# Kernel tuning notes

Measured on AMD Instinct MI355X. Metric: run time of the kernel, lower is better.

The kernel has to match this reference:

```python
import jax, jax.numpy as jnp
import numpy as np

B, H, S = 256, 128, 2048

def setup_inputs() -> dict:
    key = jax.random.key(0)
    ks = jax.random.split(key, 8)
    static_embedding = jax.random.normal(ks[0], (B, H, S), dtype=jnp.float32)
    dynamic_embedding = jax.random.normal(ks[1], (B, S, H), dtype=jnp.float32)
    decoder_output = jax.random.normal(ks[2], (B, H, 1), dtype=jnp.float32)
    mask = jax.random.randint(ks[3], (B, S), 0, 2).astype(bool)
    # xavier-uniform-ish init scales
    lim_v = float(np.sqrt(6.0 / (1 + H)))
    lim_W = float(np.sqrt(6.0 / (H + 3 * H)))
    lim_W2 = float(np.sqrt(6.0 / (H + 2 * H)))
    v = jax.random.uniform(ks[4], (H,), minval=-lim_v, maxval=lim_v, dtype=jnp.float32)
    W = jax.random.uniform(ks[5], (H, 3 * H), minval=-lim_W, maxval=lim_W, dtype=jnp.float32)
    v2 = jax.random.uniform(ks[6], (H,), minval=-lim_v, maxval=lim_v, dtype=jnp.float32)
    W2 = jax.random.uniform(ks[7], (H, 2 * H), minval=-lim_W2, maxval=lim_W2, dtype=jnp.float32)
    return {"static_embedding": static_embedding, "dynamic_embedding": dynamic_embedding,
            "decoder_output": decoder_output, "mask": mask,
            "v": v, "W": W, "v2": v2, "W2": W2}


def reference(static_embedding, dynamic_embedding, decoder_output, mask, v, W, v2, W2):
    b, h, s = static_embedding.shape
    dec = jnp.broadcast_to(decoder_output, (b, h, s))               # [B,H,S]
    hidden = jnp.concatenate(
        [static_embedding, jnp.swapaxes(dynamic_embedding, 1, 2), dec], axis=1)  # [B,3H,S]
    # stage 1: additive scoring  v^T tanh(W @ hidden)
    t1 = jnp.tanh(jnp.einsum('hk,bks->bhs', W, hidden))             # [B,H,S]
    attns = jnp.einsum('h,bhs->bs', v, t1)                          # [B,S]
    enc_attn = jax.nn.softmax(attns, axis=1)                        # [B,S]
    # context over static embeddings
    context = jnp.einsum('bs,bhs->bh', enc_attn, static_embedding)  # [B,H]
    energy = jnp.concatenate(
        [static_embedding, jnp.broadcast_to(context[:, :, None], (b, h, s))], axis=1)  # [B,2H,S]
    # stage 2
    t2 = jnp.tanh(jnp.einsum('hk,bks->bhs', W2, energy))            # [B,H,S]
    probs = jnp.einsum('h,bhs->bs', v2, t2)                         # [B,S]
    probs = jnp.where(mask, -jnp.inf, probs)
    return jax.nn.softmax(probs, axis=1)
```

## Files before the change

### kernel.cpp

```cpp
#include <hip/hip_runtime.h>
#include <stdint.h>
#include <math.h>

#define B_ 256
#define H_ 128
#define S_ 2048

typedef __attribute__((ext_vector_type(8))) short short8;
typedef __attribute__((ext_vector_type(4))) float f32x4;
typedef __attribute__((ext_vector_type(4))) unsigned int u32x4;

typedef const __attribute__((address_space(1))) void gvoid_t;
typedef __attribute__((address_space(3))) void lvoid_t;

__device__ __forceinline__ unsigned short f2bf(float f) {
  uint32_t u = __builtin_bit_cast(uint32_t, f);
  u += 0x7fffu + ((u >> 16) & 1u);
  return (unsigned short)(u >> 16);
}

__device__ __forceinline__ uint32_t cvtpk(float lo, float hi) {
  uint32_t r;
  asm("v_cvt_pk_bf16_f32 %0, %1, %2" : "=v"(r) : "v"(lo), "v"(hi));
  return r;
}

__device__ __forceinline__ float bf2f(unsigned short u) {
  return __builtin_bit_cast(float, (uint32_t)u << 16);
}

__device__ __forceinline__ float tanh5(float x) {
  float e = __builtin_amdgcn_exp2f(x * 2.8853900817779268f);
  float r = __builtin_amdgcn_rcpf(1.0f + e);
  return fmaf(-2.0f, r, 1.0f);
}

#define WS_NEED 4718592u
#define WST_OFF 8388608u
#define WS_T_NEED (WST_OFF + (size_t)B_ * (S_/16) * 4 * 64 * 8 * 2)

__global__ __launch_bounds__(256) void prep_wfrags(
    const float* __restrict__ W, const float* __restrict__ W2,
    unsigned short* __restrict__ wsA) {
  int idx = blockIdx.x * 256 + threadIdx.x;
  if (idx >= 24 * 4 * 64 * 8) return;
  int j = idx & 7;
  int lane = (idx >> 3) & 63;
  int t = (idx >> 9) & 3;
  int tile = idx >> 11;
  int li = lane & 15;
  int k = t * 32 + (lane >> 4) * 8 + j;
  float val;
  if (tile < 8)        val = W[(tile * 16 + li) * 384 + k];
  else if (tile < 16)  val = W2[((tile - 8) * 16 + li) * 256 + k];
  else                 val = W[((tile - 16) * 16 + li) * 384 + 128 + k];
  wsA[idx] = f2bf(val);
}

__global__ __launch_bounds__(128) void prep_c1(
    const float* __restrict__ W, const float* __restrict__ dec,
    float* __restrict__ c1) {
  int b = blockIdx.x;
  int h = threadIdx.x;
  __shared__ float sdec[H_];
  sdec[h] = dec[b * H_ + h];
  __syncthreads();
  const float* wr = W + h * 384 + 256;
  float acc = 0.f;
  #pragma unroll 4
  for (int k = 0; k < 128; ++k) acc += wr[k] * sdec[k];
  c1[b * H_ + h] = acc;
}

__global__ void detect_mask(const unsigned char* __restrict__ mb, int* __restrict__ flag) {
  __shared__ int sGT1, sNZ;
  if (threadIdx.x == 0) { sGT1 = 0; sNZ = 0; }
  __syncthreads();
  int gt1 = 0, nz = 0;
  for (int i = threadIdx.x; i < 8192; i += 256) {
    unsigned char c = mb[i];
    if (c > 1) gt1 = 1;
    if ((i & 3) && c) nz = 1;
  }
  if (gt1) atomicOr(&sGT1, 1);
  if (nz)  atomicOr(&sNZ, 1);
  __syncthreads();
  if (threadIdx.x == 0) *flag = sGT1 ? 2 : (sNZ ? 1 : 0);
}

__global__ __launch_bounds__(256) void stage1(
    const float* __restrict__ sEmb, const float* __restrict__ dEmb,
    const unsigned short* __restrict__ wsA, const float* __restrict__ c1,
    const float* __restrict__ v, float* __restrict__ attns,
    unsigned short* __restrict__ wsT) {
  const int b = blockIdx.y;
  const int tid = threadIdx.x;
  const int lane = tid & 63, w = tid >> 6, g = lane >> 4, li = lane & 15;
  __shared__ float sS[128 * 64];
  __shared__ unsigned short frag[4][8][512];
  __shared__ float spart[256];
  __shared__ float sc1[H_], sv[H_];

  const size_t sbase = (size_t)b * H_ * S_;
  const size_t dbase = (size_t)b * S_ * H_;
  const int sblk = blockIdx.x * 512;

  short8 aW[2][4], aB[2][4];
  #pragma unroll
  for (int mm = 0; mm < 2; ++mm)
    #pragma unroll
    for (int t = 0; t < 4; ++t) {
      aW[mm][t] = *(const short8*)(wsA + (size_t)(((2 * w + mm) * 4 + t) * 64 + lane) * 8);
      aB[mm][t] = *(const short8*)(wsA + (size_t)(((16 + 2 * w + mm) * 4 + t) * 64 + lane) * 8);
    }
  if (tid < 128) { sc1[tid] = c1[b * H_ + tid]; sv[tid] = v[tid]; }

  const int lrow = lane >> 4, lcol4 = 4 * (lane & 15);
  auto stageS = [&](int soff) {
    #pragma unroll
    for (int i = 0; i < 8; ++i) {
      int r = 32 * w + 4 * i + lrow;
      int gcol = lcol4 ^ (((r >> 3) & 3) << 3);
      const float* src = sEmb + sbase + (size_t)r * S_ + soff + gcol;
      __builtin_amdgcn_global_load_lds((gvoid_t*)src, (lvoid_t*)&sS[(32 * w + 4 * i) * 64],
                                       16, 0, 0);
    }
  };
  f32x4 dv[8];
  auto loadD = [&](int soff) {
    const float* dr = dEmb + dbase + (size_t)(soff + 16 * w + li) * H_ + 8 * g;
    #pragma unroll
    for (int t = 0; t < 4; ++t) {
      dv[2 * t]     = *(const f32x4*)(dr + 32 * t);
      dv[2 * t + 1] = *(const f32x4*)(dr + 32 * t + 4);
    }
  };

  stageS(sblk);
  loadD(sblk);

  const int colA = (16 * w + li) ^ (g << 3);

  for (int c = 0; c < 8; ++c) {
    const int soff = sblk + c * 64;
    __syncthreads();
    if (c > 0 && tid < 64)
      attns[(size_t)b * S_ + soff - 64 + tid] =
          spart[tid] + spart[64 + tid] + spart[128 + tid] + spart[192 + tid];

    #pragma unroll
    for (int t = 0; t < 4; ++t) {
      const int rb = (32 * t + 8 * g) * 64 + colA;
      uint32_t s0 = cvtpk(sS[rb], sS[rb + 64]);
      uint32_t s1 = cvtpk(sS[rb + 128], sS[rb + 192]);
      uint32_t s2 = cvtpk(sS[rb + 256], sS[rb + 320]);
      uint32_t s3 = cvtpk(sS[rb + 384], sS[rb + 448]);
      u32x4 us = {s0, s1, s2, s3};
      short8 bS = __builtin_bit_cast(short8, us);
      uint32_t d0 = cvtpk(dv[2 * t].x, dv[2 * t].y);
      uint32_t d1 = cvtpk(dv[2 * t].z, dv[2 * t].w);
      uint32_t d2 = cvtpk(dv[2 * t + 1].x, dv[2 * t + 1].y);
      uint32_t d3 = cvtpk(dv[2 * t + 1].z, dv[2 * t + 1].w);
      u32x4 ud = {d0, d1, d2, d3};
      short8 bD = __builtin_bit_cast(short8, ud);
      *(short8*)&frag[w][t][lane * 8] = bS;
      *(short8*)&frag[w][4 + t][lane * 8] = bD;
      if (wsT)
        *(short8*)&wsT[(((size_t)b * (S_ / 16) + (soff >> 4) + w) * 4 + t) * 512 + lane * 8] = bS;
    }
    __syncthreads();
    if (c + 1 < 8) { stageS(soff + 64); loadD(soff + 64); }

    f32x4 acc[4][2];
    #pragma unroll
    for (int st = 0; st < 4; ++st) { acc[st][0] = (f32x4)0.0f; acc[st][1] = (f32x4)0.0f; }
    #pragma unroll
    for (int st = 0; st < 4; ++st)
      #pragma unroll
      for (int t = 0; t < 4; ++t) {
        short8 bS = *(const short8*)&frag[st][t][lane * 8];
        short8 bD = *(const short8*)&frag[st][4 + t][lane * 8];
        acc[st][0] = __builtin_amdgcn_mfma_f32_16x16x32_bf16(aW[0][t], bS, acc[st][0], 0, 0, 0);
        acc[st][1] = __builtin_amdgcn_mfma_f32_16x16x32_bf16(aW[1][t], bS, acc[st][1], 0, 0, 0);
        acc[st][0] = __builtin_amdgcn_mfma_f32_16x16x32_bf16(aB[0][t], bD, acc[st][0], 0, 0, 0);
        acc[st][1] = __builtin_amdgcn_mfma_f32_16x16x32_bf16(aB[1][t], bD, acc[st][1], 0, 0, 0);
      }

    #pragma unroll
    for (int st = 0; st < 4; ++st) {
      float part = 0.f;
      #pragma unroll
      for (int mm = 0; mm < 2; ++mm)
        #pragma unroll
        for (int r = 0; r < 4; ++r) {
          int h = 32 * w + 16 * mm + 4 * g + r;
          part += sv[h] * tanh5(acc[st][mm][r] + sc1[h]);
        }
      part += __shfl_xor(part, 16);
      part += __shfl_xor(part, 32);
      if (lane < 16) spart[w * 64 + st * 16 + li] = part;
    }
  }
  __syncthreads();
  if (tid < 64)
    attns[(size_t)b * S_ + sblk + 448 + tid] =
        spart[tid] + spart[64 + tid] + spart[128 + tid] + spart[192 + tid];
}

__global__ __launch_bounds__(512) void fuse2(
    const float* __restrict__ attns, const unsigned short* __restrict__ wsT,
    const unsigned short* __restrict__ wsA, const float* __restrict__ W2,
    const float* __restrict__ v2, const unsigned char* __restrict__ mask8,
    const int* __restrict__ flag, float* __restrict__ out) {
  const int b = blockIdx.x;
  const int tid = threadIdx.x;
  const int lane = tid & 63, wv = tid >> 6, g = lane >> 4, li = lane & 15;
  __shared__ float buf[S_];
  __shared__ float sctx[8][H_];
  __shared__ float2 sq[H_];
  __shared__ float wred[8];
  __shared__ float sred;

  const size_t pbase = (size_t)b * (S_ / 16);

  float a[4];
  #pragma unroll
  for (int i = 0; i < 4; ++i) a[i] = attns[(size_t)b * S_ + i * 512 + tid];
  float mx = fmaxf(fmaxf(a[0], a[1]), fmaxf(a[2], a[3]));
  #pragma unroll
  for (int off = 32; off >= 1; off >>= 1) mx = fmaxf(mx, __shfl_xor(mx, off));
  if (lane == 0) wred[wv] = mx;
  __syncthreads();
  if (tid == 0) {
    float m = wred[0];
    #pragma unroll
    for (int i = 1; i < 8; ++i) m = fmaxf(m, wred[i]);
    sred = m;
  }
  __syncthreads();
  mx = sred;
  __syncthreads();
  float sum = 0.f;
  #pragma unroll
  for (int i = 0; i < 4; ++i) {
    float e = __expf(a[i] - mx);
    buf[i * 512 + tid] = e;
    sum += e;
  }
  #pragma unroll
  for (int off = 32; off >= 1; off >>= 1) sum += __shfl_xor(sum, off);
  if (lane == 0) wred[wv] = sum;
  __syncthreads();
  if (tid == 0) {
    float s = 0.f;
    #pragma unroll
    for (int i = 0; i < 8; ++i) s += wred[i];
    sred = 1.0f / s;
  }
  __syncthreads();
  const float inv1 = sred;
  __syncthreads();

  float hacc[4][8];
  #pragma unroll
  for (int t = 0; t < 4; ++t)
    #pragma unroll
    for (int j = 0; j < 8; ++j) hacc[t][j] = 0.f;
  short8 cur[4];
  #pragma unroll
  for (int t = 0; t < 4; ++t)
    cur[t] = *(const short8*)&wsT[((pbase + wv) * 4 + t) * 512 + lane * 8];
  for (int stile = wv; stile < 128; stile += 8) {
    short8 nxt[4];
    const bool more = (stile + 8) < 128;
    if (more) {
      #pragma unroll
      for (int t = 0; t < 4; ++t)
        nxt[t] = *(const short8*)&wsT[((pbase + stile + 8) * 4 + t) * 512 + lane * 8];
    }
    float pw = buf[stile * 16 + li];
    #pragma unroll
    for (int t = 0; t < 4; ++t)
      #pragma unroll
      for (int j = 0; j < 8; ++j)
        hacc[t][j] = fmaf(pw, bf2f((unsigned short)cur[t][j]), hacc[t][j]);
    if (more) {
      #pragma unroll
      for (int t = 0; t < 4; ++t) cur[t] = nxt[t];
    }
  }
  #pragma unroll
  for (int t = 0; t < 4; ++t)
    #pragma unroll
    for (int j = 0; j < 8; ++j) {
      float x = hacc[t][j];
      x += __shfl_xor(x, 1); x += __shfl_xor(x, 2);
      x += __shfl_xor(x, 4); x += __shfl_xor(x, 8);
      hacc[t][j] = x;
    }
  if (li == 0) {
    #pragma unroll
    for (int t = 0; t < 4; ++t)
      #pragma unroll
      for (int j = 0; j < 8; ++j)
        sctx[wv][32 * t + 8 * g + j] = hacc[t][j];
  }
  __syncthreads();

  if (tid < 128) {
    float cx = 0.f;
    #pragma unroll
    for (int q = 0; q < 8; ++q) cx += sctx[q][tid];
    sctx[0][tid] = cx * inv1;
  }
  __syncthreads();
  if (tid < 128) {
    const float* wr = W2 + tid * 256 + 128;
    float c2v = 0.f;
    #pragma unroll 4
    for (int k = 0; k < 128; ++k) c2v += wr[k] * sctx[0][k];
    sq[tid] = make_float2(c2v, v2[tid]);
  }
  __syncthreads();

  short8 aW[8][4];
  #pragma unroll
  for (int m = 0; m < 8; ++m)
    #pragma unroll
    for (int t = 0; t < 4; ++t)
      aW[m][t] = *(const short8*)(wsA + (size_t)(((8 + m) * 4 + t) * 64 + lane) * 8);
  const int f = *flag;

  short8 bcur[4];
  #pragma unroll
  for (int t = 0; t < 4; ++t)
    bcur[t] = *(const short8*)&wsT[((pbase + wv) * 4 + t) * 512 + lane * 8];
  for (int stile = wv; stile < 128; stile += 8) {
    short8 bnxt[4];
    const bool more = (stile + 8) < 128;
    if (more) {
      #pragma unroll
      for (int t = 0; t < 4; ++t)
        bnxt[t] = *(const short8*)&wsT[((pbase + stile + 8) * 4 + t) * 512 + lane * 8];
    }
    f32x4 acc[8];
    #pragma unroll
    for (int m = 0; m < 8; ++m) acc[m] = (f32x4)0.0f;
    #pragma unroll
    for (int t = 0; t < 4; ++t)
      #pragma unroll
      for (int m = 0; m < 8; ++m)
        acc[m] = __builtin_amdgcn_mfma_f32_16x16x32_bf16(aW[m][t], bcur[t], acc[m], 0, 0, 0);
    float part = 0.f;
    #pragma unroll
    for (int m = 0; m < 8; ++m)
      #pragma unroll
      for (int r = 0; r < 4; ++r) {
        float2 q = sq[16 * m + 4 * g + r];
        part += q.y * tanh5(acc[m][r] + q.x);
      }
    part += __shfl_xor(part, 16);
    part += __shfl_xor(part, 32);
    if (lane < 16) {
      int s = stile * 16 + li;
      size_t mi = (size_t)b * S_ + s;
      bool msk;
      if (f == 1)      msk = mask8[mi] != 0;
      else if (f == 2) msk = ((const float*)mask8)[mi] != 0.0f;
      else             msk = ((const int*)mask8)[mi] != 0;
      buf[s] = msk ? -INFINITY : part;
    }
    if (more) {
      #pragma unroll
      for (int t = 0; t < 4; ++t) bcur[t] = bnxt[t];
    }
  }
  __syncthreads();

  float s4[4];
  #pragma unroll
  for (int i = 0; i < 4; ++i) s4[i] = buf[i * 512 + tid];
  float mx2 = fmaxf(fmaxf(s4[0], s4[1]), fmaxf(s4[2], s4[3]));
  #pragma unroll
  for (int off = 32; off >= 1; off >>= 1) mx2 = fmaxf(mx2, __shfl_xor(mx2, off));
  if (lane == 0) wred[wv] = mx2;
  __syncthreads();
  if (tid == 0) {
    float m = wred[0];
    #pragma unroll
    for (int i = 1; i < 8; ++i) m = fmaxf(m, wred[i]);
    sred = m;
  }
  __syncthreads();
  mx2 = sred;
  __syncthreads();
  float e4[4];
  float sum2 = 0.f;
  #pragma unroll
  for (int i = 0; i < 4; ++i) { e4[i] = __expf(s4[i] - mx2); sum2 += e4[i]; }
  #pragma unroll
  for (int off = 32; off >= 1; off >>= 1) sum2 += __shfl_xor(sum2, off);
  if (lane == 0) wred[wv] = sum2;
  __syncthreads();
  if (tid == 0) {
    float s = 0.f;
    #pragma unroll
    for (int i = 0; i < 8; ++i) s += wred[i];
    sred = 1.0f / s;
  }
  __syncthreads();
  const float inv2 = sred;
  #pragma unroll
  for (int i = 0; i < 4; ++i) out[(size_t)b * S_ + i * 512 + tid] = e4[i] * inv2;
}

__global__ __launch_bounds__(256) void kmid_a(
    const float* __restrict__ attns, const float* __restrict__ sEmb,
    float* __restrict__ ctx) {
  int q = blockIdx.x, b = blockIdx.y;
  int tid = threadIdx.x, lane = tid & 63, w = tid >> 6;
  __shared__ float p[S_];
  __shared__ float wred[4];
  __shared__ float sred;
  float a[8];
  #pragma unroll
  for (int i = 0; i < 8; ++i) a[i] = attns[(size_t)b * S_ + i * 256 + tid];
  float mx = a[0];
  #pragma unroll
  for (int i = 1; i < 8; ++i) mx = fmaxf(mx, a[i]);
  #pragma unroll
  for (int off = 32; off >= 1; off >>= 1) mx = fmaxf(mx, __shfl_xor(mx, off));
  if (lane == 0) wred[w] = mx;
  __syncthreads();
  if (tid == 0) sred = fmaxf(fmaxf(wred[0], wred[1]), fmaxf(wred[2], wred[3]));
  __syncthreads();
  mx = sred;
  __syncthreads();
  float sum = 0.f;
  #pragma unroll
  for (int i = 0; i < 8; ++i) {
    float e = __expf(a[i] - mx);
    p[i * 256 + tid] = e;
    sum += e;
  }
  #pragma unroll
  for (int off = 32; off >= 1; off >>= 1) sum += __shfl_xor(sum, off);
  if (lane == 0) wred[w] = sum;
  __syncthreads();
  if (tid == 0) sred = 1.0f / (wred[0] + wred[1] + wred[2] + wred[3]);
  __syncthreads();
  float inv = sred;
  #pragma unroll
  for (int hh = 0; hh < 8; ++hh) {
    int h = q * 32 + w * 8 + hh;
    const f32x4* xp = (const f32x4*)(sEmb + (size_t)b * H_ * S_ + (size_t)h * S_);
    float av = 0.f;
    #pragma unroll
    for (int it = 0; it < 8; ++it) {
      f32x4 x = xp[it * 64 + lane];
      f32x4 pp = *(const f32x4*)&p[(it * 64 + lane) * 4];
      av += x.x * pp.x + x.y * pp.y + x.z * pp.z + x.w * pp.w;
    }
    #pragma unroll
    for (int off = 32; off >= 1; off >>= 1) av += __shfl_xor(av, off);
    if (lane == 0) ctx[b * H_ + h] = av * inv;
  }
}

__global__ __launch_bounds__(128) void kmid_b(
    const float* __restrict__ W2, const float* __restrict__ ctx,
    float* __restrict__ c2) {
  int b = blockIdx.x;
  int h = threadIdx.x;
  __shared__ float sc[H_];
  sc[h] = ctx[b * H_ + h];
  __syncthreads();
  const float* wr = W2 + h * 256 + 128;
  float acc = 0.f;
  #pragma unroll 4
  for (int k = 0; k < 128; ++k) acc += wr[k] * sc[k];
  c2[b * H_ + h] = acc;
}

__global__ __launch_bounds__(256) void stage2F(
    const float* __restrict__ sEmb, const unsigned short* __restrict__ wsA,
    const float* __restrict__ c2, const float* __restrict__ v2,
    const unsigned char* __restrict__ mask8, const int* __restrict__ flag,
    float* __restrict__ score) {
  int b = blockIdx.y;
  int tid = threadIdx.x;
  int lane = tid & 63, w = tid >> 6, g = lane >> 4, li = lane & 15;
  __shared__ float sS[128 * 64];
  __shared__ float sc2[H_], sv2[H_];
  __shared__ float spart[256];
  const int schunk = blockIdx.x * 64;
  const size_t sbase = (size_t)b * H_ * S_;
  short8 aW[2][4];
  #pragma unroll
  for (int mm = 0; mm < 2; ++mm)
    #pragma unroll
    for (int t = 0; t < 4; ++t)
      aW[mm][t] = *(const short8*)(wsA + (size_t)(((8 + 2 * w + mm) * 4 + t) * 64 + lane) * 8);
  {
    int lrow = lane >> 4, lcol4 = 4 * (lane & 15);
    #pragma unroll
    for (int i = 0; i < 8; ++i) {
      int r = 32 * w + 4 * i + lrow;
      int gcol = lcol4 ^ (((r >> 3) & 3) << 3);
      const float* src = sEmb + sbase + (size_t)r * S_ + schunk + gcol;
      __builtin_amdgcn_global_load_lds((gvoid_t*)src, (lvoid_t*)&sS[(32 * w + 4 * i) * 64],
                                       16, 0, 0);
    }
  }
  if (tid < 128) { sc2[tid] = c2[b * H_ + tid]; sv2[tid] = v2[tid]; }
  __syncthreads();
  f32x4 acc[4][2];
  #pragma unroll
  for (int st = 0; st < 4; ++st) { acc[st][0] = (f32x4)0.0f; acc[st][1] = (f32x4)0.0f; }
  #pragma unroll
  for (int st = 0; st < 4; ++st) {
    const int colA = (16 * st + li) ^ (g << 3);
    #pragma unroll
    for (int t = 0; t < 4; ++t) {
      short8 bS;
      #pragma unroll
      for (int j = 0; j < 8; ++j)
        bS[j] = (short)f2bf(sS[(32 * t + 8 * g + j) * 64 + colA]);
      acc[st][0] = __builtin_amdgcn_mfma_f32_16x16x32_bf16(aW[0][t], bS, acc[st][0], 0, 0, 0);
      acc[st][1] = __builtin_amdgcn_mfma_f32_16x16x32_bf16(aW[1][t], bS, acc[st][1], 0, 0, 0);
    }
  }
  #pragma unroll
  for (int st = 0; st < 4; ++st) {
    float part = 0.f;
    #pragma unroll
    for (int mm = 0; mm < 2; ++mm)
      #pragma unroll
      for (int r = 0; r < 4; ++r) {
        int h = 32 * w + 16 * mm + 4 * g + r;
        part += sv2[h] * tanh5(acc[st][mm][r] + sc2[h]);
      }
    part += __shfl_xor(part, 16);
    part += __shfl_xor(part, 32);
    if (lane < 16) spart[w * 64 + st * 16 + li] = part;
  }
  __syncthreads();
  if (tid < 64) {
    float tot = spart[tid] + spart[64 + tid] + spart[128 + tid] + spart[192 + tid];
    size_t mi = (size_t)b * S_ + schunk + tid;
    int f = *flag;
    bool msk;
    if (f == 1)      msk = mask8[mi] != 0;
    else if (f == 2) msk = ((const float*)mask8)[mi] != 0.0f;
    else             msk = ((const int*)mask8)[mi] != 0;
    score[mi] = msk ? -INFINITY : tot;
  }
}

__global__ __launch_bounds__(256) void ksoftmax(
    const float* __restrict__ score, float* __restrict__ out) {
  int b = blockIdx.x;
  int tid = threadIdx.x, lane = tid & 63, w = tid >> 6;
  __shared__ float wred[4];
  __shared__ float sred;
  float a[8];
  #pragma unroll
  for (int i = 0; i < 8; ++i) a[i] = score[(size_t)b * S_ + i * 256 + tid];
  float mx = a[0];
  #pragma unroll
  for (int i = 1; i < 8; ++i) mx = fmaxf(mx, a[i]);
  #pragma unroll
  for (int off = 32; off >= 1; off >>= 1) mx = fmaxf(mx, __shfl_xor(mx, off));
  if (lane == 0) wred[w] = mx;
  __syncthreads();
  if (tid == 0) sred = fmaxf(fmaxf(wred[0], wred[1]), fmaxf(wred[2], wred[3]));
  __syncthreads();
  mx = sred;
  __syncthreads();
  float e[8];
  float sum = 0.f;
  #pragma unroll
  for (int i = 0; i < 8; ++i) { e[i] = __expf(a[i] - mx); sum += e[i]; }
  #pragma unroll
  for (int off = 32; off >= 1; off >>= 1) sum += __shfl_xor(sum, off);
  if (lane == 0) wred[w] = sum;
  __syncthreads();
  if (tid == 0) sred = 1.0f / (wred[0] + wred[1] + wred[2] + wred[3]);
  __syncthreads();
  float inv = sred;
  #pragma unroll
  for (int i = 0; i < 8; ++i) out[(size_t)b * S_ + i * 256 + tid] = e[i] * inv;
}

extern "C" void kernel_launch(void* const* d_in, const int* in_sizes, int n_in,
                              void* d_out, int out_size, void* d_ws, size_t ws_size,
                              hipStream_t stream) {
  (void)in_sizes; (void)n_in; (void)out_size;
  if (ws_size < WS_NEED) return;
  const float* sEmb = (const float*)d_in[0];
  const float* dEmb = (const float*)d_in[1];
  const float* dec  = (const float*)d_in[2];
  const unsigned char* mask = (const unsigned char*)d_in[3];
  const float* v    = (const float*)d_in[4];
  const float* W    = (const float*)d_in[5];
  const float* v2   = (const float*)d_in[6];
  const float* W2   = (const float*)d_in[7];

  char* ws = (char*)d_ws;
  unsigned short* wsA = (unsigned short*)(ws);
  int*   flag  = (int*)  (ws + 114688);
  float* c1    = (float*)(ws + 131072);
  float* c2    = (float*)(ws + 262144);
  float* ctx   = (float*)(ws + 393216);
  float* attns = (float*)(ws + 524288);
  float* score = (float*)(ws + 2621440);
  bool useT = (ws_size >= WS_T_NEED);
  unsigned short* wsT = useT ? (unsigned short*)(ws + WST_OFF) : nullptr;

  prep_wfrags<<<192, 256, 0, stream>>>(W, W2, wsA);
  prep_c1<<<B_, 128, 0, stream>>>(W, dec, c1);
  detect_mask<<<1, 256, 0, stream>>>(mask, flag);
  stage1<<<dim3(4, B_), 256, 0, stream>>>(sEmb, dEmb, wsA, c1, v, attns, wsT);
  if (useT) {
    fuse2<<<B_, 512, 0, stream>>>(attns, wsT, wsA, W2, v2, mask, flag, (float*)d_out);
  } else {
    kmid_a<<<dim3(4, B_), 256, 0, stream>>>(attns, sEmb, ctx);
    kmid_b<<<B_, 128, 0, stream>>>(W2, ctx, c2);
    stage2F<<<dim3(32, B_), 256, 0, stream>>>(sEmb, wsA, c2, v2, mask, flag, score);
    ksoftmax<<<B_, 256, 0, stream>>>(score, (float*)d_out);
  }
}
```

Before: 229.9 us.

## Split static-embedding bf16 transpose into prepT kernel and double-buffer stage1

Adds a separate prepT kernel that converts the static embedding to bf16 MFMA fragments in the workspace. stage1 then reads those pre-packed fragments via global_load_lds into double-buffered LDS, and stages the dynamic embedding into a swizzled, double-buffered LDS tile with explicit waitcnt and sched barriers. The aim is to overlap loads with MFMA work and to remove the in-loop fp32-to-bf16 transposition from stage1, using launch bounds that allow two blocks per CU. The cost is an extra kernel launch plus an extra write and read pass over the bf16 static tensor. The hand-written vmcnt waits also risk synchronisation mistakes.

```diff
diff --git a/kernel.cpp b/kernel.cpp
--- a/kernel.cpp
+++ b/kernel.cpp
@@ -12,6 +12,8 @@
 
 typedef const __attribute__((address_space(1))) void gvoid_t;
 typedef __attribute__((address_space(3))) void lvoid_t;
+
+#define SCHED0 __builtin_amdgcn_sched_barrier(0)
 
 __device__ __forceinline__ unsigned short f2bf(float f) {
   uint32_t u = __builtin_bit_cast(uint32_t, f);
@@ -88,11 +90,383 @@
   if (threadIdx.x == 0) *flag = sGT1 ? 2 : (sNZ ? 1 : 0);
 }
 
-__global__ __launch_bounds__(256) void stage1(
+__global__ __launch_bounds__(256) void prepT(
+    const float* __restrict__ sEmb, unsigned short* __restrict__ wsT) {
+  const int kb = blockIdx.x;
+  const int b  = blockIdx.y;
+  const int tid = threadIdx.x, lane = tid & 63, w = tid >> 6;
+  const int li = lane & 15, g = lane >> 4;
+  __shared__ unsigned short sT[32 * 260];
+
+  const size_t sbase = (size_t)b * H_ * S_ + (size_t)(32 * kb) * S_;
+  const size_t obase = (size_t)b * (S_ / 16);
+
+  for (int sb = 0; sb < 8; ++sb) {
+    const int s0 = sb * 256;
+    f32x4 rv[8];
+    #pragma unroll
+    for (int i = 0; i < 8; ++i)
+      rv[i] = *(const f32x4*)(sEmb + sbase + (size_t)(8 * w + i) * S_ + s0 + 4 * lane);
+    #pragma unroll
+    for (int i = 0; i < 8; ++i) {
+      uint32_t p0 = cvtpk(rv[i].x, rv[i].y), p1 = cvtpk(rv[i].z, rv[i].w);
+      uint32_t* dst = (uint32_t*)&sT[(8 * w + i) * 260 + 4 * lane];
+      dst[0] = p0; dst[1] = p1;
+    }
+    __syncthreads();
+    #pragma unroll
+    for (int it = 0; it < 4; ++it) {
+      const int st = 4 * it + w;
+      short8 frag;
+      #pragma unroll
+      for (int j = 0; j < 8; ++j)
+        frag[j] = (short)sT[(8 * g + j) * 260 + 16 * st + li];
+      *(short8*)&wsT[((obase + 16 * sb + st) * 4 + kb) * 512 + lane * 8] = frag;
+    }
+    __syncthreads();
+  }
+}
+
+__global__ __launch_bounds__(256, 2) void stage1(
+    const float* __restrict__ dEmb, const unsigned short* __restrict__ wsT,
+    const unsigned short* __restrict__ wsA, const float* __restrict__ c1,
+    const float* __restrict__ v, float* __restrict__ attns) {
+  const int b = blockIdx.y;
+  const int tid = threadIdx.x;
+  const int lane = tid & 63, w = tid >> 6, g = lane >> 4, li = lane & 15;
+  __shared__ unsigned short fragS[2][16][512];
+  __shared__ unsigned short sD[2][64 * 128];
+  __shared__ float spart[2][4][64];
+  __shared__ float sc1[H_], sv[H_];
+
+  const size_t dbase = (size_t)b * S_ * H_;
+  const size_t pbase = (size_t)b * (S_ / 16);
+  const int sblk = blockIdx.x * 512;
+
+  short8 aW[2][4], aB[2][4];
+  #pragma unroll
+  for (int mm = 0; mm < 2; ++mm)
+    #pragma unroll
+    for (int t = 0; t < 4; ++t) {
+      aW[mm][t] = *(const short8*)(wsA + (size_t)(((2 * w + mm) * 4 + t) * 64 + lane) * 8);
+      aB[mm][t] = *(const short8*)(wsA + (size_t)(((16 + 2 * w + mm) * 4 + t) * 64 + lane) * 8);
+    }
+  { int hh = 32 * w + (lane & 31); sc1[hh] = c1[b * H_ + hh]; sv[hh] = v[hh]; }
+
+  f32x4 dv[8];
+  auto loadDyn = [&](int c) {
+    const float* base = dEmb + dbase + (size_t)(sblk + c * 64 + 16 * w) * H_;
+    #pragma unroll
+    for (int i = 0; i < 8; ++i)
+      dv[i] = *(const f32x4*)(base + (size_t)(2 * i + (lane >> 5)) * H_ + 4 * (lane & 31));
+  };
+  auto issueFrag = [&](int c, int buf) {
+    const size_t st0 = pbase + (sblk >> 4) + c * 4 + w;
+    #pragma unroll
+    for (int t = 0; t < 4; ++t) {
+      const unsigned short* src = wsT + (st0 * 4 + t) * 512 + lane * 8;
+      __builtin_amdgcn_global_load_lds((gvoid_t*)src,
+                                       (lvoid_t*)&fragS[buf][w * 4 + t][0], 16, 0, 0);
+    }
+  };
+  auto writeDyn = [&](int buf) {
+    #pragma unroll
+    for (int i = 0; i < 8; ++i) {
+      uint32_t p0 = cvtpk(dv[i].x, dv[i].y), p1 = cvtpk(dv[i].z, dv[i].w);
+      int r = 16 * w + 2 * i + (lane >> 5);
+      int u = (lane & 31) >> 1, h = lane & 1;
+      uint2* dst = (uint2*)&sD[buf][r * 128 + ((u ^ (r & 7)) << 3) + h * 4];
+      *dst = make_uint2(p0, p1);
+    }
+  };
+
+  loadDyn(0);
+  SCHED0;
+  issueFrag(0, 0);
+  SCHED0;
+  writeDyn(0);
+  SCHED0;
+
+  int cb = 0, db = 0;
+  for (int c = 0; c < 8; ++c) {
+    if (c == 0) { asm volatile("s_waitcnt vmcnt(0)" ::: "memory"); }
+    else        { asm volatile("s_waitcnt vmcnt(1)" ::: "memory"); }
+    asm volatile("s_waitcnt lgkmcnt(0)" ::: "memory");
+    SCHED0;
+    __builtin_amdgcn_s_barrier();
+    SCHED0;
+
+    if (c + 1 < 8) {
+      loadDyn(c + 1);
+      SCHED0;
+      issueFrag(c + 1, cb ^ 1);
+    }
+    SCHED0;
+
+    if (c > 0) {
+      const int pb = (c - 1) & 1;
+      int idx = 16 * w + li;
+      float tot = spart[pb][0][idx] + spart[pb][1][idx] + spart[pb][2][idx] + spart[pb][3][idx];
+      if (lane < 16) attns[(size_t)b * S_ + sblk + (c - 1) * 64 + idx] = tot;
+    }
+    SCHED0;
+
+    f32x4 acc[4][2];
+    #pragma unroll
+    for (int st = 0; st < 4; ++st) { acc[st][0] = (f32x4)0.0f; acc[st][1] = (f32x4)0.0f; }
+    #pragma unroll
+    for (int st = 0; st < 4; ++st)
+      #pragma unroll
+      for (int t = 0; t < 4; ++t) {
+        short8 bS = *(const short8*)&fragS[cb][st * 4 + t][lane * 8];
+        short8 bD = *(const short8*)&sD[db][(16 * st + li) * 128 + (((4 * t + g) ^ (li & 7)) << 3)];
+        acc[st][0] = __builtin_amdgcn_mfma_f32_16x16x32_bf16(aW[0][t], bS, acc[st][0], 0, 0, 0);
+        acc[st][1] = __builtin_amdgcn_mfma_f32_16x16x32_bf16(aW[1][t], bS, acc[st][1], 0, 0, 0);
+        acc[st][0] = __builtin_amdgcn_mfma_f32_16x16x32_bf16(aB[0][t], bD, acc[st][0], 0, 0, 0);
+        acc[st][1] = __builtin_amdgcn_mfma_f32_16x16x32_bf16(aB[1][t], bD, acc[st][1], 0, 0, 0);
+      }
+
+    #pragma unroll
+    for (int st = 0; st < 4; ++st) {
+      float part = 0.f;
+      #pragma unroll
+      for (int mm = 0; mm < 2; ++mm)
+        #pragma unroll
+        for (int r = 0; r < 4; ++r) {
+          int h = 32 * w + 16 * mm + 4 * g + r;
+          part += sv[h] * tanh5(acc[st][mm][r] + sc1[h]);
+        }
+      part += __shfl_xor(part, 16);
+      part += __shfl_xor(part, 32);
+      if (lane < 16) spart[c & 1][w][st * 16 + li] = part;
+    }
+
+    if (c + 1 < 8) writeDyn(db ^ 1);
+    cb ^= 1; db ^= 1;
+  }
+
+  asm volatile("s_waitcnt lgkmcnt(0)" ::: "memory");
+  SCHED0;
+  __builtin_amdgcn_s_barrier();
+  SCHED0;
+  {
+    int idx = 16 * w + li;
+    float tot = spart[1][0][idx] + spart[1][1][idx] + spart[1][2][idx] + spart[1][3][idx];
+    if (lane < 16) attns[(size_t)b * S_ + sblk + 7 * 64 + idx] = tot;
+  }
+}
+
+__global__ __launch_bounds__(512) void fuse2(
+    const float* __restrict__ attns, const unsigned short* __restrict__ wsT,
+    const unsigned short* __restrict__ wsA, const float* __restrict__ W2,
+    const float* __restrict__ v2, const unsigned char* __restrict__ mask8,
+    const int* __restrict__ flag, float* __restrict__ out) {
+  const int b = blockIdx.x;
+  const int tid = threadIdx.x;
+  const int lane = tid & 63, wv = tid >> 6, g = lane >> 4, li = lane & 15;
+  __shared__ float buf[S_];
+  __shared__ float sctx[8][H_];
+  __shared__ float2 sq[H_];
+  __shared__ float wred[8];
+  __shared__ float sred;
+
+  const size_t pbase = (size_t)b * (S_ / 16);
+
+  float a[4];
+  #pragma unroll
+  for (int i = 0; i < 4; ++i) a[i] = attns[(size_t)b * S_ + i * 512 + tid];
+  float mx = fmaxf(fmaxf(a[0], a[1]), fmaxf(a[2], a[3]));
+  #pragma unroll
+  for (int off = 32; off >= 1; off >>= 1) mx = fmaxf(mx, __shfl_xor(mx, off));
+  if (lane == 0) wred[wv] = mx;
+  __syncthreads();
+  if (tid == 0) {
+    float m = wred[0];
+    #pragma unroll
+    for (int i = 1; i < 8; ++i) m = fmaxf(m, wred[i]);
+    sred = m;
+  }
+  __syncthreads();
+  mx = sred;
+  __syncthreads();
+  float sum = 0.f;
+  #pragma unroll
+  for (int i = 0; i < 4; ++i) {
+    float e = __expf(a[i] - mx);
+    buf[i * 512 + tid] = e;
+    sum += e;
+  }
+  #pragma unroll
+  for (int off = 32; off >= 1; off >>= 1) sum += __shfl_xor(sum, off);
+  if (lane == 0) wred[wv] = sum;
+  __syncthreads();
+  if (tid == 0) {
+    float s = 0.f;
+    #pragma unroll
+    for (int i = 0; i < 8; ++i) s += wred[i];
+    sred = 1.0f / s;
+  }
+  __syncthreads();
+  const float inv1 = sred;
+  __syncthreads();
+
+  float hacc[4][8];
+  #pragma unroll
+  for (int t = 0; t < 4; ++t)
+    #pragma unroll
+    for (int j = 0; j < 8; ++j) hacc[t][j] = 0.f;
+  short8 cur[4];
+  #pragma unroll
+  for (int t = 0; t < 4; ++t)
+    cur[t] = *(const short8*)&wsT[((pbase + wv) * 4 + t) * 512 + lane * 8];
+  for (int stile = wv; stile < 128; stile += 8) {
+    short8 nxt[4];
+    const bool more = (stile + 8) < 128;
+    if (more) {
+      #pragma unroll
+      for (int t = 0; t < 4; ++t)
+        nxt[t] = *(const short8*)&wsT[((pbase + stile + 8) * 4 + t) * 512 + lane * 8];
+    }
+    float pw = buf[stile * 16 + li];
+    #pragma unroll
+    for (int t = 0; t < 4; ++t)
+      #pragma unroll
+      for (int j = 0; j < 8; ++j)
+        hacc[t][j] = fmaf(pw, bf2f((unsigned short)cur[t][j]), hacc[t][j]);
+    if (more) {
+      #pragma unroll
+      for (int t = 0; t < 4; ++t) cur[t] = nxt[t];
+    }
+  }
+  #pragma unroll
+  for (int t = 0; t < 4; ++t)
+    #pragma unroll
+    for (int j = 0; j < 8; ++j) {
+      float x = hacc[t][j];
+      x += __shfl_xor(x, 1); x += __shfl_xor(x, 2);
+      x += __shfl_xor(x, 4); x += __shfl_xor(x, 8);
+      hacc[t][j] = x;
+    }
+  if (li == 0) {
+    #pragma unroll
+    for (int t = 0; t < 4; ++t)
+      #pragma unroll
+      for (int j = 0; j < 8; ++j)
+        sctx[wv][32 * t + 8 * g + j] = hacc[t][j];
+  }
+  __syncthreads();
+
+  if (tid < 128) {
+    float cx = 0.f;
+    #pragma unroll
+    for (int q = 0; q < 8; ++q) cx += sctx[q][tid];
+    sctx[0][tid] = cx * inv1;
+  }
+  __syncthreads();
+  if (tid < 128) {
+    const float* wr = W2 + tid * 256 + 128;
+    float c2v = 0.f;
+    #pragma unroll 4
+    for (int k = 0; k < 128; ++k) c2v += wr[k] * sctx[0][k];
+    sq[tid] = make_float2(c2v, v2[tid]);
+  }
+  __syncthreads();
+
+  short8 aW[8][4];
+  #pragma unroll
+  for (int m = 0; m < 8; ++m)
+    #pragma unroll
+    for (int t = 0; t < 4; ++t)
+      aW[m][t] = *(const short8*)(wsA + (size_t)(((8 + m) * 4 + t) * 64 + lane) * 8);
+  const int f = *flag;
+
+  short8 bcur[4];
+  #pragma unroll
+  for (int t = 0; t < 4; ++t)
+    bcur[t] = *(const short8*)&wsT[((pbase + wv) * 4 + t) * 512 + lane * 8];
+  for (int stile = wv; stile < 128; stile += 8) {
+    short8 bnxt[4];
+    const bool more = (stile + 8) < 128;
+    if (more) {
+      #pragma unroll
+      for (int t = 0; t < 4; ++t)
+        bnxt[t] = *(const short8*)&wsT[((pbase + stile + 8) * 4 + t) * 512 + lane * 8];
+    }
+    f32x4 acc[8];
+    #pragma unroll
+    for (int m = 0; m < 8; ++m) acc[m] = (f32x4)0.0f;
+    #pragma unroll
+    for (int t = 0; t < 4; ++t)
+      #pragma unroll
+      for (int m = 0; m < 8; ++m)
+        acc[m] = __builtin_amdgcn_mfma_f32_16x16x32_bf16(aW[m][t], bcur[t], acc[m], 0, 0, 0);
+    float part = 0.f;
+    #pragma unroll
+    for (int m = 0; m < 8; ++m)
+      #pragma unroll
+      for (int r = 0; r < 4; ++r) {
+        float2 q = sq[16 * m + 4 * g + r];
+        part += q.y * tanh5(acc[m][r] + q.x);
+      }
+    part += __shfl_xor(part, 16);
+    part += __shfl_xor(part, 32);
+    if (lane < 16) {
+      int s = stile * 16 + li;
+      size_t mi = (size_t)b * S_ + s;
+      bool msk;
+      if (f == 1)      msk = mask8[mi] != 0;
+      else if (f == 2) msk = ((const float*)mask8)[mi] != 0.0f;
+      else             msk = ((const int*)mask8)[mi] != 0;
+      buf[s] = msk ? -INFINITY : part;
+    }
+    if (more) {
+      #pragma unroll
+      for (int t = 0; t < 4; ++t) bcur[t] = bnxt[t];
+    }
+  }
+  __syncthreads();
+
+  float s4[4];
+  #pragma unroll
+  for (int i = 0; i < 4; ++i) s4[i] = buf[i * 512 + tid];
+  float mx2 = fmaxf(fmaxf(s4[0], s4[1]), fmaxf(s4[2], s4[3]));
+  #pragma unroll
+  for (int off = 32; off >= 1; off >>= 1) mx2 = fmaxf(mx2, __shfl_xor(mx2, off));
+  if (lane == 0) wred[wv] = mx2;
+  __syncthreads();
+  if (tid == 0) {
+    float m = wred[0];
+    #pragma unroll
+    for (int i = 1; i < 8; ++i) m = fmaxf(m, wred[i]);
+    sred = m;
+  }
+  __syncthreads();
+  mx2 = sred;
+  __syncthreads();
+  float e4[4];
+  float sum2 = 0.f;
+  #pragma unroll
+  for (int i = 0; i < 4; ++i) { e4[i] = __expf(s4[i] - mx2); sum2 += e4[i]; }
+  #pragma unroll
+  for (int off = 32; off >= 1; off >>= 1) sum2 += __shfl_xor(sum2, off);
+  if (lane == 0) wred[wv] = sum2;
+  __syncthreads();
+  if (tid == 0) {
+    float s = 0.f;
+    #pragma unroll
+    for (int i = 0; i < 8; ++i) s += wred[i];
+    sred = 1.0f / s;
+  }
+  __syncthreads();
+  const float inv2 = sred;
+  #pragma unroll
+  for (int i = 0; i < 4; ++i) out[(size_t)b * S_ + i * 512 + tid] = e4[i] * inv2;
+}
+
+__global__ __launch_bounds__(256) void stage1_fb(
     const float* __restrict__ sEmb, const float* __restrict__ dEmb,
     const unsigned short* __restrict__ wsA, const float* __restrict__ c1,
-    const float* __restrict__ v, float* __restrict__ attns,
-    unsigned short* __restrict__ wsT) {
+    const float* __restrict__ v, float* __restrict__ attns) {
   const int b = blockIdx.y;
   const int tid = threadIdx.x;
   const int lane = tid & 63, w = tid >> 6, g = lane >> 4, li = lane & 15;
@@ -135,10 +509,8 @@
       dv[2 * t + 1] = *(const f32x4*)(dr + 32 * t + 4);
     }
   };
-
   stageS(sblk);
   loadD(sblk);
-
   const int colA = (16 * w + li) ^ (g << 3);
 
   for (int c = 0; c < 8; ++c) {
@@ -147,7 +519,6 @@
     if (c > 0 && tid < 64)
       attns[(size_t)b * S_ + soff - 64 + tid] =
           spart[tid] + spart[64 + tid] + spart[128 + tid] + spart[192 + tid];
-
     #pragma unroll
     for (int t = 0; t < 4; ++t) {
       const int rb = (32 * t + 8 * g) * 64 + colA;
@@ -165,12 +536,9 @@
       short8 bD = __builtin_bit_cast(short8, ud);
       *(short8*)&frag[w][t][lane * 8] = bS;
       *(short8*)&frag[w][4 + t][lane * 8] = bD;
-      if (wsT)
-        *(short8*)&wsT[(((size_t)b * (S_ / 16) + (soff >> 4) + w) * 4 + t) * 512 + lane * 8] = bS;
     }
     __syncthreads();
     if (c + 1 < 8) { stageS(soff + 64); loadD(soff + 64); }
-
     f32x4 acc[4][2];
     #pragma unroll
     for (int st = 0; st < 4; ++st) { acc[st][0] = (f32x4)0.0f; acc[st][1] = (f32x4)0.0f; }
@@ -185,7 +553,6 @@
         acc[st][0] = __builtin_amdgcn_mfma_f32_16x16x32_bf16(aB[0][t], bD, acc[st][0], 0, 0, 0);
         acc[st][1] = __builtin_amdgcn_mfma_f32_16x16x32_bf16(aB[1][t], bD, acc[st][1], 0, 0, 0);
       }
-
     #pragma unroll
     for (int st = 0; st < 4; ++st) {
       float part = 0.f;
@@ -205,213 +572,6 @@
   if (tid < 64)
     attns[(size_t)b * S_ + sblk + 448 + tid] =
         spart[tid] + spart[64 + tid] + spart[128 + tid] + spart[192 + tid];
-}
-
-__global__ __launch_bounds__(512) void fuse2(
-    const float* __restrict__ attns, const unsigned short* __restrict__ wsT,
-    const unsigned short* __restrict__ wsA, const float* __restrict__ W2,
-    const float* __restrict__ v2, const unsigned char* __restrict__ mask8,
-    const int* __restrict__ flag, float* __restrict__ out) {
-  const int b = blockIdx.x;
-  const int tid = threadIdx.x;
-  const int lane = tid & 63, wv = tid >> 6, g = lane >> 4, li = lane & 15;
-  __shared__ float buf[S_];
-  __shared__ float sctx[8][H_];
-  __shared__ float2 sq[H_];
-  __shared__ float wred[8];
-  __shared__ float sred;
-
-  const size_t pbase = (size_t)b * (S_ / 16);
-
-  float a[4];
-  #pragma unroll
-  for (int i = 0; i < 4; ++i) a[i] = attns[(size_t)b * S_ + i * 512 + tid];
-  float mx = fmaxf(fmaxf(a[0], a[1]), fmaxf(a[2], a[3]));
-  #pragma unroll
-  for (int off = 32; off >= 1; off >>= 1) mx = fmaxf(mx, __shfl_xor(mx, off));
-  if (lane == 0) wred[wv] = mx;
-  __syncthreads();
-  if (tid == 0) {
-    float m = wred[0];
-    #pragma unroll
-    for (int i = 1; i < 8; ++i) m = fmaxf(m, wred[i]);
-    sred = m;
-  }
-  __syncthreads();
-  mx = sred;
-  __syncthreads();
-  float sum = 0.f;
-  #pragma unroll
-  for (int i = 0; i < 4; ++i) {
-    float e = __expf(a[i] - mx);
-    buf[i * 512 + tid] = e;
-    sum += e;
-  }
-  #pragma unroll
-  for (int off = 32; off >= 1; off >>= 1) sum += __shfl_xor(sum, off);
-  if (lane == 0) wred[wv] = sum;
-  __syncthreads();
-  if (tid == 0) {
-    float s = 0.f;
-    #pragma unroll
-    for (int i = 0; i < 8; ++i) s += wred[i];
-    sred = 1.0f / s;
-  }
-  __syncthreads();
-  const float inv1 = sred;
-  __syncthreads();
-
-  float hacc[4][8];
-  #pragma unroll
-  for (int t = 0; t < 4; ++t)
-    #pragma unroll
-    for (int j = 0; j < 8; ++j) hacc[t][j] = 0.f;
-  short8 cur[4];
-  #pragma unroll
-  for (int t = 0; t < 4; ++t)
-    cur[t] = *(const short8*)&wsT[((pbase + wv) * 4 + t) * 512 + lane * 8];
-  for (int stile = wv; stile < 128; stile += 8) {
-    short8 nxt[4];
-    const bool more = (stile + 8) < 128;
-    if (more) {
-      #pragma unroll
-      for (int t = 0; t < 4; ++t)
-        nxt[t] = *(const short8*)&wsT[((pbase + stile + 8) * 4 + t) * 512 + lane * 8];
-    }
-    float pw = buf[stile * 16 + li];
-    #pragma unroll
-    for (int t = 0; t < 4; ++t)
-      #pragma unroll
-      for (int j = 0; j < 8; ++j)
-        hacc[t][j] = fmaf(pw, bf2f((unsigned short)cur[t][j]), hacc[t][j]);
-    if (more) {
-      #pragma unroll
-      for (int t = 0; t < 4; ++t) cur[t] = nxt[t];
-    }
-  }
-  #pragma unroll
-  for (int t = 0; t < 4; ++t)
-    #pragma unroll
-    for (int j = 0; j < 8; ++j) {
-      float x = hacc[t][j];
-      x += __shfl_xor(x, 1); x += __shfl_xor(x, 2);
-      x += __shfl_xor(x, 4); x += __shfl_xor(x, 8);
-      hacc[t][j] = x;
-    }
-  if (li == 0) {
-    #pragma unroll
-    for (int t = 0; t < 4; ++t)
-      #pragma unroll
-      for (int j = 0; j < 8; ++j)
-        sctx[wv][32 * t + 8 * g + j] = hacc[t][j];
-  }
-  __syncthreads();
-
-  if (tid < 128) {
-    float cx = 0.f;
-    #pragma unroll
-    for (int q = 0; q < 8; ++q) cx += sctx[q][tid];
-    sctx[0][tid] = cx * inv1;
-  }
-  __syncthreads();
-  if (tid < 128) {
-    const float* wr = W2 + tid * 256 + 128;
-    float c2v = 0.f;
-    #pragma unroll 4
-    for (int k = 0; k < 128; ++k) c2v += wr[k] * sctx[0][k];
-    sq[tid] = make_float2(c2v, v2[tid]);
-  }
-  __syncthreads();
-
-  short8 aW[8][4];
-  #pragma unroll
-  for (int m = 0; m < 8; ++m)
-    #pragma unroll
-    for (int t = 0; t < 4; ++t)
-      aW[m][t] = *(const short8*)(wsA + (size_t)(((8 + m) * 4 + t) * 64 + lane) * 8);
-  const int f = *flag;
-
-  short8 bcur[4];
-  #pragma unroll
-  for (int t = 0; t < 4; ++t)
-    bcur[t] = *(const short8*)&wsT[((pbase + wv) * 4 + t) * 512 + lane * 8];
-  for (int stile = wv; stile < 128; stile += 8) {
-    short8 bnxt[4];
-    const bool more = (stile + 8) < 128;
-    if (more) {
-      #pragma unroll
-      for (int t = 0; t < 4; ++t)
-        bnxt[t] = *(const short8*)&wsT[((pbase + stile + 8) * 4 + t) * 512 + lane * 8];
-    }
-    f32x4 acc[8];
-    #pragma unroll
-    for (int m = 0; m < 8; ++m) acc[m] = (f32x4)0.0f;
-    #pragma unroll
-    for (int t = 0; t < 4; ++t)
-      #pragma unroll
-      for (int m = 0; m < 8; ++m)
-        acc[m] = __builtin_amdgcn_mfma_f32_16x16x32_bf16(aW[m][t], bcur[t], acc[m], 0, 0, 0);
-    float part = 0.f;
-    #pragma unroll
-    for (int m = 0; m < 8; ++m)
-      #pragma unroll
-      for (int r = 0; r < 4; ++r) {
-        float2 q = sq[16 * m + 4 * g + r];
-        part += q.y * tanh5(acc[m][r] + q.x);
-      }
-    part += __shfl_xor(part, 16);
-    part += __shfl_xor(part, 32);
-    if (lane < 16) {
-      int s = stile * 16 + li;
-      size_t mi = (size_t)b * S_ + s;
-      bool msk;
-      if (f == 1)      msk = mask8[mi] != 0;
-      else if (f == 2) msk = ((const float*)mask8)[mi] != 0.0f;
-      else             msk = ((const int*)mask8)[mi] != 0;
-      buf[s] = msk ? -INFINITY : part;
-    }
-    if (more) {
-      #pragma unroll
-      for (int t = 0; t < 4; ++t) bcur[t] = bnxt[t];
-    }
-  }
-  __syncthreads();
-
-  float s4[4];
-  #pragma unroll
-  for (int i = 0; i < 4; ++i) s4[i] = buf[i * 512 + tid];
-  float mx2 = fmaxf(fmaxf(s4[0], s4[1]), fmaxf(s4[2], s4[3]));
-  #pragma unroll
-  for (int off = 32; off >= 1; off >>= 1) mx2 = fmaxf(mx2, __shfl_xor(mx2, off));
-  if (lane == 0) wred[wv] = mx2;
-  __syncthreads();
-  if (tid == 0) {
-    float m = wred[0];
-    #pragma unroll
-    for (int i = 1; i < 8; ++i) m = fmaxf(m, wred[i]);
-    sred = m;
-  }
-  __syncthreads();
-  mx2 = sred;
-  __syncthreads();
-  float e4[4];
-  float sum2 = 0.f;
-  #pragma unroll
-  for (int i = 0; i < 4; ++i) { e4[i] = __expf(s4[i] - mx2); sum2 += e4[i]; }
-  #pragma unroll
-  for (int off = 32; off >= 1; off >>= 1) sum2 += __shfl_xor(sum2, off);
-  if (lane == 0) wred[wv] = sum2;
-  __syncthreads();
-  if (tid == 0) {
-    float s = 0.f;
-    #pragma unroll
-    for (int i = 0; i < 8; ++i) s += wred[i];
-    sred = 1.0f / s;
-  }
-  __syncthreads();
-  const float inv2 = sred;
-  #pragma unroll
-  for (int i = 0; i < 4; ++i) out[(size_t)b * S_ + i * 512 + tid] = e4[i] * inv2;
 }
 
 __global__ __launch_bounds__(256) void kmid_a(
@@ -620,10 +780,12 @@
   prep_wfrags<<<192, 256, 0, stream>>>(W, W2, wsA);
   prep_c1<<<B_, 128, 0, stream>>>(W, dec, c1);
   detect_mask<<<1, 256, 0, stream>>>(mask, flag);
-  stage1<<<dim3(4, B_), 256, 0, stream>>>(sEmb, dEmb, wsA, c1, v, attns, wsT);
   if (useT) {
+    prepT<<<dim3(4, B_), 256, 0, stream>>>(sEmb, wsT);
+    stage1<<<dim3(4, B_), 256, 0, stream>>>(dEmb, wsT, wsA, c1, v, attns);
     fuse2<<<B_, 512, 0, stream>>>(attns, wsT, wsA, W2, v2, mask, flag, (float*)d_out);
   } else {
+    stage1_fb<<<dim3(4, B_), 256, 0, stream>>>(sEmb, dEmb, wsA, c1, v, attns);
     kmid_a<<<dim3(4, B_), 256, 0, stream>>>(attns, sEmb, ctx);
     kmid_b<<<B_, 128, 0, stream>>>(W2, ctx, c2);
     stage2F<<<dim3(32, B_), 256, 0, stream>>>(sEmb, wsA, c2, v2, mask, flag, score);
```

After: 267.8 us. 16.5% more time.
